# Kernel tuning notes

Measured on AMD Instinct MI355X. Metric: run time of the kernel, lower is better.

## Reference

```python
import jax, jax.numpy as jnp
import numpy as np


def _integral(x):
    # x: [C, H, W] -> summed-area table [C, H+1, W+1] with zero first row/col
    s = jnp.cumsum(jnp.cumsum(x, axis=-2), axis=-1)
    return jnp.pad(s, ((0, 0), (1, 0), (1, 0)))


def _box_sums(S, x0, y0, x1, y1):
    # S: [C, H+1, W+1]; boxes half-open [y0:y1, x0:x1] -> sums [C, N]
    return S[:, y1, x1] - S[:, y0, x1] - S[:, y1, x0] + S[:, y0, x0]


def setup_inputs() -> dict:
    key = jax.random.key(0)
    C, H, W, K, N = 256, 512, 512, 21, 2560
    k1, k2, k3, k4, k5, k6, k7 = jax.random.split(key, 7)
    feature_map = jax.random.normal(k1, (C, H, W), dtype=jnp.float32)
    norm_cam_bg = jax.random.uniform(k2, (K, H, W), dtype=jnp.float32)
    # valid crop boxes (xmin, ymin, xmax, ymax) with 8..64 px extent
    x0 = jax.random.randint(k3, (N,), 0, W - 64)
    y0 = jax.random.randint(k4, (N,), 0, H - 64)
    bw = jax.random.randint(k5, (N,), 8, 64)
    bh = jax.random.randint(k6, (N,), 8, 64)
    boxes = jnp.stack([x0, y0, x0 + bw, y0 + bh], axis=1).astype(jnp.int32)
    labels = jax.random.randint(k7, (N,), 0, K).astype(jnp.int32)
    return {"feature_map": feature_map, "norm_cam_bg": norm_cam_bg,
            "boxes": boxes, "labels": labels}


def reference(feature_map, norm_cam_bg, boxes, labels):
    # feature_map: [C, H, W]; norm_cam_bg: [K, H, W]; boxes: [N, 4] int; labels: [N] int
    K = norm_cam_bg.shape[0]
    N = boxes.shape[0]
    x0, y0, x1, y1 = boxes[:, 0], boxes[:, 1], boxes[:, 2], boxes[:, 3]
    area = ((x1 - x0) * (y1 - y0)).astype(feature_map.dtype)  # [N]

    # per-box adaptive_avg_pool2d(region, (1,1)) == mean over region, via integral image
    S = _integral(feature_map)                                # [C, H+1, W+1]
    pool = _box_sums(S, x0, y0, x1, y1).T / area[:, None]     # [N, C]

    # foreground score: fraction of pixels in box where argmax(CAM) == region label
    cam_predict = jnp.argmax(norm_cam_bg, axis=0)             # [H, W]
    onehot = jax.nn.one_hot(cam_predict, K, dtype=feature_map.dtype)  # [H, W, K]
    Sm = _integral(jnp.moveaxis(onehot, -1, 0))               # [K, H+1, W+1]
    fg_sums = _box_sums(Sm, x0, y0, x1, y1)                   # [K, N]
    fg_score = fg_sums[labels, jnp.arange(N)] / area          # [N]

    return pool, fg_score
```

## Files before the change

### kernel.cpp

```cpp
#include <hip/hip_runtime.h>

#define HWD (512*512)
#define Wd 512
#define Hd 512
#define Cd 256
#define Kd 21
#define Nd 2560
#define NSTRIP 4
#define SROWS 128

__global__ __launch_bounds__(512) void k_events(const int* __restrict__ boxes,
                                                int* __restrict__ ev_start,
                                                unsigned int* __restrict__ ev_list) {
    __shared__ int cnt[512];
    __shared__ int cur[512];
    __shared__ int tt[8];
    const int t = threadIdx.x, lane = t & 63, wv = t >> 6;
    cnt[t] = 0;
    __syncthreads();
    for (int n = t; n < Nd; n += 512) {
        const int y0 = boxes[n * 4 + 1];
        const int y1 = boxes[n * 4 + 3];
        if (y0 > 0) atomicAdd(&cnt[y0 - 1], 1);
        atomicAdd(&cnt[y1 - 1], 1);
    }
    __syncthreads();
    const int v = cnt[t];
    int inc = v;
    #pragma unroll
    for (int d = 1; d < 64; d <<= 1) {
        int u = __shfl_up(inc, d);
        if (lane >= d) inc += u;
    }
    if (lane == 63) tt[wv] = inc;
    __syncthreads();
    int off = 0;
    #pragma unroll
    for (int w = 0; w < 8; ++w) if (w < wv) off += tt[w];
    inc += off;
    cur[t] = inc - v;
    ev_start[t] = inc - v;
    if (t == 511) ev_start[512] = inc;
    __syncthreads();
    for (int n = t; n < Nd; n += 512) {
        const int y0 = boxes[n * 4 + 1];
        const int y1 = boxes[n * 4 + 3];
        if (y0 > 0) {
            const int r = y0 - 1;
            const int p = atomicAdd(&cur[r], 1);
            ev_list[p] = (unsigned)n | ((unsigned)r << 12) | 0x80000000u;
        }
        const int r = y1 - 1;
        const int p = atomicAdd(&cur[r], 1);
        ev_list[p] = (unsigned)n | ((unsigned)r << 12);
    }
}

__global__ __launch_bounds__(512) void k_ipool(const float* __restrict__ f,
                                               const int* __restrict__ boxes,
                                               const int* __restrict__ ev_start,
                                               const unsigned int* __restrict__ ev_list,
                                               float* __restrict__ pool_acc) {
    const int c     = blockIdx.x >> 2;
    const int strip = blockIdx.x & 3;
    const int t = threadIdx.x;
    const int lane = t & 63, wv = t >> 6;
    const float* F = f + (size_t)c * HWD + (size_t)(strip * SROWS) * Wd;

    __shared__ float S[8][512];
    __shared__ float partial[Nd];

    for (int n = t; n < Nd; n += 512) partial[n] = 0.f;

    float colacc = 0.f;
    const float* rp = F + (size_t)wv * Wd + lane * 8;
    float4 a = *(const float4*)(rp);
    float4 b = *(const float4*)(rp + 4);

    for (int yb = 0; yb < SROWS; yb += 8) {
        const bool more = (yb + 8 < SROWS);
        float4 na, nb;
        if (more) {
            const float* np = F + (size_t)(yb + 8 + wv) * Wd + lane * 8;
            na = *(const float4*)(np);
            nb = *(const float4*)(np + 4);
        }

        float v0 = a.x, v1 = v0 + a.y, v2 = v1 + a.z, v3 = v2 + a.w;
        float v4 = v3 + b.x, v5 = v4 + b.y, v6 = v5 + b.z, v7 = v6 + b.w;
        float s = v7, xx = s;
        #pragma unroll
        for (int d = 1; d < 64; d <<= 1) {
            float u = __shfl_up(xx, d);
            if (lane >= d) xx += u;
        }
        const float off = xx - s;
        float4 o0 = { v0 + off, v1 + off, v2 + off, v3 + off };
        float4 o1 = { v4 + off, v5 + off, v6 + off, v7 + off };
        *(float4*)&S[wv][lane * 8]     = o0;
        *(float4*)&S[wv][lane * 8 + 4] = o1;
        __syncthreads();

        #pragma unroll
        for (int j = 0; j < 8; ++j) {
            colacc += S[j][t];
            S[j][t] = colacc;
        }
        __syncthreads();

        const int g0 = strip * SROWS + yb;
        const int e0 = ev_start[g0];
        const int e1 = ev_start[g0 + 8];
        for (int e = e0 + t; e < e1; e += 512) {
            const unsigned ev = ev_list[e];
            const int n  = ev & 0xFFF;
            const int r  = (ev >> 12) & 0x1FF;
            const int x0 = boxes[n * 4 + 0];
            const int x1 = boxes[n * 4 + 2];
            const float sx1 = S[r & 7][x1 - 1];
            const float sx0 = (x0 > 0) ? S[r & 7][x0 - 1] : 0.f;
            const float d = sx1 - sx0;
            partial[n] += (ev & 0x80000000u) ? -d : d;
        }
        __syncthreads();

        if (more) { a = na; b = nb; }
    }

    S[0][t] = colacc;
    __syncthreads();
    for (int n = t; n < Nd; n += 512) {
        const int x0 = boxes[n * 4 + 0];
        const int y0 = boxes[n * 4 + 1];
        const int x1 = boxes[n * 4 + 2];
        const int y1 = boxes[n * 4 + 3];
        float p = partial[n];
        const float tdiff = S[0][x1 - 1] - ((x0 > 0) ? S[0][x0 - 1] : 0.f);
        if (strip < ((y1 - 1) >> 7)) p += tdiff;
        if (y0 > 0 && strip < ((y0 - 1) >> 7)) p -= tdiff;
        pool_acc[((size_t)(strip * Cd + c)) * Nd + n] = p;
    }
}

__global__ __launch_bounds__(512) void k_pool2(const float* __restrict__ pool_acc,
                                               const int* __restrict__ boxes,
                                               float* __restrict__ pool) {
    __shared__ float P[32][257];
    __shared__ float rarea[32];
    const int t = threadIdx.x;
    const int n0 = blockIdx.x * 32;

    if (t < 32) {
        const int x0 = boxes[(n0 + t) * 4 + 0];
        const int y0 = boxes[(n0 + t) * 4 + 1];
        const int x1 = boxes[(n0 + t) * 4 + 2];
        const int y1 = boxes[(n0 + t) * 4 + 3];
        rarea[t] = 1.f / (float)((x1 - x0) * (y1 - y0));
    }

    const int ni = t & 31, ci = t >> 5;
    #pragma unroll
    for (int co = 0; co < 16; ++co) {
        const int c = co * 16 + ci;
        float v = 0.f;
        #pragma unroll
        for (int s = 0; s < NSTRIP; ++s)
            v += pool_acc[((size_t)(s * Cd + c)) * Nd + n0 + ni];
        P[ni][c] = v;
    }
    __syncthreads();

    const int c = t & 255, nn = t >> 8;
    #pragma unroll
    for (int no = 0; no < 16; ++no) {
        const int i = no * 2 + nn;
        pool[(size_t)(n0 + i) * Cd + c] = P[i][c] * rarea[i];
    }
}

__global__ __launch_bounds__(256) void k_argmax(const float* __restrict__ ncb,
                                                unsigned char* __restrict__ map) {
    const int p = blockIdx.x * 256 + threadIdx.x;
    float best = ncb[p];
    int bi = 0;
    #pragma unroll
    for (int k = 1; k < Kd; ++k) {
        float v = ncb[(size_t)k * HWD + p];
        if (v > best) { best = v; bi = k; }
    }
    map[p] = (unsigned char)bi;
}

__global__ __launch_bounds__(256) void k_fg(const unsigned char* __restrict__ map,
                                            const int* __restrict__ boxes,
                                            const int* __restrict__ labels,
                                            float* __restrict__ fg) {
    const int n = blockIdx.x;
    const int x0 = boxes[n * 4 + 0];
    const int y0 = boxes[n * 4 + 1];
    const int x1 = boxes[n * 4 + 2];
    const int y1 = boxes[n * 4 + 3];
    const int lab = labels[n];
    const int lane = threadIdx.x & 63;
    const int wv   = threadIdx.x >> 6;
    const int w = x1 - x0;

    int cnt = 0;
    for (int yy = y0 + wv; yy < y1; yy += 4) {
        if (lane < w)
            cnt += (map[yy * Wd + x0 + lane] == lab) ? 1 : 0;
    }
    #pragma unroll
    for (int d = 32; d; d >>= 1) cnt += __shfl_down(cnt, d);

    __shared__ int sred[4];
    if (lane == 0) sred[wv] = cnt;
    __syncthreads();
    if (threadIdx.x == 0) {
        int tot = sred[0] + sred[1] + sred[2] + sred[3];
        float area = (float)(w * (y1 - y0));
        fg[n] = (float)tot / area;
    }
}

extern "C" void kernel_launch(void* const* d_in, const int* in_sizes, int n_in,
                              void* d_out, int out_size, void* d_ws, size_t ws_size,
                              hipStream_t stream) {
    (void)in_sizes; (void)n_in; (void)out_size; (void)ws_size;

    const float* feature_map = (const float*)d_in[0];
    const float* norm_cam_bg = (const float*)d_in[1];
    const int*   boxes       = (const int*)d_in[2];
    const int*   labels      = (const int*)d_in[3];

    float* out_pool = (float*)d_out;
    float* out_fg   = out_pool + (size_t)Nd * Cd;

    char* ws = (char*)d_ws;
    unsigned char* map      = (unsigned char*)ws;
    int*           ev_start = (int*)(ws + 262144);
    unsigned int*  ev_list  = (unsigned int*)(ws + 266240);
    float*         pool_acc = (float*)(ws + 286720);

    k_events<<<1, 512, 0, stream>>>(boxes, ev_start, ev_list);
    k_argmax<<<HWD / 256, 256, 0, stream>>>(norm_cam_bg, map);
    k_ipool<<<Cd * NSTRIP, 512, 0, stream>>>(feature_map, boxes, ev_start, ev_list,
                                             pool_acc);
    k_pool2<<<Nd / 32, 512, 0, stream>>>(pool_acc, boxes, out_pool);
    k_fg<<<Nd, 256, 0, stream>>>(map, boxes, labels, out_fg);
}
```

Measured before the change: 79.97 us.

## Merge argmax into integral-pool kernel and fg into pool-finalize kernel

The argmax pass now runs as extra blocks of the integral-pool kernel, and the foreground-count pass runs as extra blocks of the pool-finalize kernel, with one box per wave. This cuts five launches to three and lets independent work share the GPU. The pool kernel also drops the in-shared column prefix rewrite and its second barrier per 8-row block. Instead it keeps a double-buffered running column sum and has event threads add up the needed rows themselves, which adds a little per-event work. The launch bound raises the occupancy hint to 8 blocks.

```diff
diff --git a/kernel.cpp b/kernel.cpp
--- a/kernel.cpp
+++ b/kernel.cpp
@@ -56,23 +56,43 @@
     }
 }
 
-__global__ __launch_bounds__(512) void k_ipool(const float* __restrict__ f,
-                                               const int* __restrict__ boxes,
-                                               const int* __restrict__ ev_start,
-                                               const unsigned int* __restrict__ ev_list,
-                                               float* __restrict__ pool_acc) {
-    const int c     = blockIdx.x >> 2;
-    const int strip = blockIdx.x & 3;
+__global__ __launch_bounds__(512, 8) void kA(const float* __restrict__ f,
+                                             const int* __restrict__ boxes,
+                                             const int* __restrict__ ev_start,
+                                             const unsigned int* __restrict__ ev_list,
+                                             const float* __restrict__ ncb,
+                                             unsigned char* __restrict__ map,
+                                             float* __restrict__ pool_acc) {
+    const int bid = blockIdx.x;
     const int t = threadIdx.x;
+
+    if (bid >= Cd * NSTRIP) {
+        const int p = (bid - Cd * NSTRIP) * 512 + t;
+        float best = ncb[p];
+        int bi = 0;
+        #pragma unroll
+        for (int k = 1; k < Kd; ++k) {
+            float v = ncb[(size_t)k * HWD + p];
+            if (v > best) { best = v; bi = k; }
+        }
+        map[p] = (unsigned char)bi;
+        return;
+    }
+
+    const int c     = bid >> 2;
+    const int strip = bid & 3;
     const int lane = t & 63, wv = t >> 6;
     const float* F = f + (size_t)c * HWD + (size_t)(strip * SROWS) * Wd;
 
     __shared__ float S[8][512];
+    __shared__ float C[2][512];
     __shared__ float partial[Nd];
 
     for (int n = t; n < Nd; n += 512) partial[n] = 0.f;
+    C[0][t] = 0.f;
 
     float colacc = 0.f;
+    int buf = 0;
     const float* rp = F + (size_t)wv * Wd + lane * 8;
     float4 a = *(const float4*)(rp);
     float4 b = *(const float4*)(rp + 4);
@@ -101,12 +121,11 @@
         *(float4*)&S[wv][lane * 8 + 4] = o1;
         __syncthreads();
 
-        #pragma unroll
-        for (int j = 0; j < 8; ++j) {
-            colacc += S[j][t];
-            S[j][t] = colacc;
-        }
-        __syncthreads();
+        float cs = 0.f;
+        #pragma unroll
+        for (int j = 0; j < 8; ++j) cs += S[j][t];
+        colacc += cs;
+        C[buf ^ 1][t] = colacc;
 
         const int g0 = strip * SROWS + yb;
         const int e0 = ev_start[g0];
@@ -114,113 +133,95 @@
         for (int e = e0 + t; e < e1; e += 512) {
             const unsigned ev = ev_list[e];
             const int n  = ev & 0xFFF;
-            const int r  = (ev >> 12) & 0x1FF;
+            const int rr = (ev >> 12) & 7;
             const int x0 = boxes[n * 4 + 0];
             const int x1 = boxes[n * 4 + 2];
-            const float sx1 = S[r & 7][x1 - 1];
-            const float sx0 = (x0 > 0) ? S[r & 7][x0 - 1] : 0.f;
+            float sx1 = C[buf][x1 - 1];
+            float sx0 = (x0 > 0) ? C[buf][x0 - 1] : 0.f;
+            for (int j = 0; j <= rr; ++j) {
+                sx1 += S[j][x1 - 1];
+                if (x0 > 0) sx0 += S[j][x0 - 1];
+            }
             const float d = sx1 - sx0;
             partial[n] += (ev & 0x80000000u) ? -d : d;
         }
         __syncthreads();
 
+        buf ^= 1;
         if (more) { a = na; b = nb; }
     }
 
-    S[0][t] = colacc;
-    __syncthreads();
     for (int n = t; n < Nd; n += 512) {
         const int x0 = boxes[n * 4 + 0];
         const int y0 = boxes[n * 4 + 1];
         const int x1 = boxes[n * 4 + 2];
         const int y1 = boxes[n * 4 + 3];
         float p = partial[n];
-        const float tdiff = S[0][x1 - 1] - ((x0 > 0) ? S[0][x0 - 1] : 0.f);
+        const float tdiff = C[buf][x1 - 1] - ((x0 > 0) ? C[buf][x0 - 1] : 0.f);
         if (strip < ((y1 - 1) >> 7)) p += tdiff;
         if (y0 > 0 && strip < ((y0 - 1) >> 7)) p -= tdiff;
         pool_acc[((size_t)(strip * Cd + c)) * Nd + n] = p;
     }
 }
 
-__global__ __launch_bounds__(512) void k_pool2(const float* __restrict__ pool_acc,
-                                               const int* __restrict__ boxes,
-                                               float* __restrict__ pool) {
-    __shared__ float P[32][257];
-    __shared__ float rarea[32];
+__global__ __launch_bounds__(512) void kB(const float* __restrict__ pool_acc,
+                                          const unsigned char* __restrict__ map,
+                                          const int* __restrict__ boxes,
+                                          const int* __restrict__ labels,
+                                          float* __restrict__ pool,
+                                          float* __restrict__ fg) {
+    const int bid = blockIdx.x;
     const int t = threadIdx.x;
-    const int n0 = blockIdx.x * 32;
-
-    if (t < 32) {
-        const int x0 = boxes[(n0 + t) * 4 + 0];
-        const int y0 = boxes[(n0 + t) * 4 + 1];
-        const int x1 = boxes[(n0 + t) * 4 + 2];
-        const int y1 = boxes[(n0 + t) * 4 + 3];
-        rarea[t] = 1.f / (float)((x1 - x0) * (y1 - y0));
-    }
-
-    const int ni = t & 31, ci = t >> 5;
-    #pragma unroll
-    for (int co = 0; co < 16; ++co) {
-        const int c = co * 16 + ci;
-        float v = 0.f;
-        #pragma unroll
-        for (int s = 0; s < NSTRIP; ++s)
-            v += pool_acc[((size_t)(s * Cd + c)) * Nd + n0 + ni];
-        P[ni][c] = v;
-    }
-    __syncthreads();
-
-    const int c = t & 255, nn = t >> 8;
-    #pragma unroll
-    for (int no = 0; no < 16; ++no) {
-        const int i = no * 2 + nn;
-        pool[(size_t)(n0 + i) * Cd + c] = P[i][c] * rarea[i];
-    }
-}
-
-__global__ __launch_bounds__(256) void k_argmax(const float* __restrict__ ncb,
-                                                unsigned char* __restrict__ map) {
-    const int p = blockIdx.x * 256 + threadIdx.x;
-    float best = ncb[p];
-    int bi = 0;
-    #pragma unroll
-    for (int k = 1; k < Kd; ++k) {
-        float v = ncb[(size_t)k * HWD + p];
-        if (v > best) { best = v; bi = k; }
-    }
-    map[p] = (unsigned char)bi;
-}
-
-__global__ __launch_bounds__(256) void k_fg(const unsigned char* __restrict__ map,
-                                            const int* __restrict__ boxes,
-                                            const int* __restrict__ labels,
-                                            float* __restrict__ fg) {
-    const int n = blockIdx.x;
+
+    if (bid < Nd / 32) {
+        __shared__ float P[32][257];
+        __shared__ float rarea[32];
+        const int n0 = bid * 32;
+        if (t < 32) {
+            const int x0 = boxes[(n0 + t) * 4 + 0];
+            const int y0 = boxes[(n0 + t) * 4 + 1];
+            const int x1 = boxes[(n0 + t) * 4 + 2];
+            const int y1 = boxes[(n0 + t) * 4 + 3];
+            rarea[t] = 1.f / (float)((x1 - x0) * (y1 - y0));
+        }
+        const int ni = t & 31, ci = t >> 5;
+        #pragma unroll
+        for (int co = 0; co < 16; ++co) {
+            const int c = co * 16 + ci;
+            float v = 0.f;
+            #pragma unroll
+            for (int s = 0; s < NSTRIP; ++s)
+                v += pool_acc[((size_t)(s * Cd + c)) * Nd + n0 + ni];
+            P[ni][c] = v;
+        }
+        __syncthreads();
+        const int c = t & 255, nn = t >> 8;
+        #pragma unroll
+        for (int no = 0; no < 16; ++no) {
+            const int i = no * 2 + nn;
+            pool[(size_t)(n0 + i) * Cd + c] = P[i][c] * rarea[i];
+        }
+        return;
+    }
+
+    const int lane = t & 63, wv = t >> 6;
+    const int n = (bid - Nd / 32) * 8 + wv;
     const int x0 = boxes[n * 4 + 0];
     const int y0 = boxes[n * 4 + 1];
     const int x1 = boxes[n * 4 + 2];
     const int y1 = boxes[n * 4 + 3];
     const int lab = labels[n];
-    const int lane = threadIdx.x & 63;
-    const int wv   = threadIdx.x >> 6;
     const int w = x1 - x0;
 
     int cnt = 0;
-    for (int yy = y0 + wv; yy < y1; yy += 4) {
+    for (int yy = y0; yy < y1; ++yy) {
         if (lane < w)
             cnt += (map[yy * Wd + x0 + lane] == lab) ? 1 : 0;
     }
     #pragma unroll
     for (int d = 32; d; d >>= 1) cnt += __shfl_down(cnt, d);
-
-    __shared__ int sred[4];
-    if (lane == 0) sred[wv] = cnt;
-    __syncthreads();
-    if (threadIdx.x == 0) {
-        int tot = sred[0] + sred[1] + sred[2] + sred[3];
-        float area = (float)(w * (y1 - y0));
-        fg[n] = (float)tot / area;
-    }
+    if (lane == 0)
+        fg[n] = (float)cnt / (float)(w * (y1 - y0));
 }
 
 extern "C" void kernel_launch(void* const* d_in, const int* in_sizes, int n_in,
@@ -243,9 +244,8 @@
     float*         pool_acc = (float*)(ws + 286720);
 
     k_events<<<1, 512, 0, stream>>>(boxes, ev_start, ev_list);
-    k_argmax<<<HWD / 256, 256, 0, stream>>>(norm_cam_bg, map);
-    k_ipool<<<Cd * NSTRIP, 512, 0, stream>>>(feature_map, boxes, ev_start, ev_list,
-                                             pool_acc);
-    k_pool2<<<Nd / 32, 512, 0, stream>>>(pool_acc, boxes, out_pool);
-    k_fg<<<Nd, 256, 0, stream>>>(map, boxes, labels, out_fg);
-}
+    kA<<<Cd * NSTRIP + HWD / 512, 512, 0, stream>>>(feature_map, boxes, ev_start,
+                                                    ev_list, norm_cam_bg, map, pool_acc);
+    kB<<<Nd / 32 + Nd / 8, 512, 0, stream>>>(pool_acc, map, boxes, labels,
+                                             out_pool, out_fg);
+}
```

After: 89.39 us. 1.12x slower.

## Fuse argmax and event-building kernels; prefetch two row-blocks ahead in ipool

Applied to the files above, without the earlier changes.

Merges the argmax kernel and the single-block event-sorting kernel into one launch, with block 512 doing event construction while the other blocks compute the CAM argmax. This removes one kernel launch and lets the serial event kernel overlap with the argmax work. In the integral-pool kernel the feature rows are now prefetched two 8-row blocks ahead instead of one, to hide more global-load latency at the cost of extra registers. The column-scan reads are also batched into registers before the scan.

```diff
diff --git a/kernel.cpp b/kernel.cpp
--- a/kernel.cpp
+++ b/kernel.cpp
@@ -9,13 +9,29 @@
 #define NSTRIP 4
 #define SROWS 128
 
-__global__ __launch_bounds__(512) void k_events(const int* __restrict__ boxes,
-                                                int* __restrict__ ev_start,
-                                                unsigned int* __restrict__ ev_list) {
+__global__ __launch_bounds__(512) void k_pre(const float* __restrict__ ncb,
+                                             const int* __restrict__ boxes,
+                                             unsigned char* __restrict__ map,
+                                             int* __restrict__ ev_start,
+                                             unsigned int* __restrict__ ev_list) {
+    const int t = threadIdx.x;
+    if (blockIdx.x < 512) {
+        const int p = blockIdx.x * 512 + t;
+        float best = ncb[p];
+        int bi = 0;
+        #pragma unroll
+        for (int k = 1; k < Kd; ++k) {
+            float v = ncb[(size_t)k * HWD + p];
+            if (v > best) { best = v; bi = k; }
+        }
+        map[p] = (unsigned char)bi;
+        return;
+    }
+
     __shared__ int cnt[512];
     __shared__ int cur[512];
     __shared__ int tt[8];
-    const int t = threadIdx.x, lane = t & 63, wv = t >> 6;
+    const int lane = t & 63, wv = t >> 6;
     cnt[t] = 0;
     __syncthreads();
     for (int n = t; n < Nd; n += 512) {
@@ -73,21 +89,25 @@
     for (int n = t; n < Nd; n += 512) partial[n] = 0.f;
 
     float colacc = 0.f;
-    const float* rp = F + (size_t)wv * Wd + lane * 8;
-    float4 a = *(const float4*)(rp);
-    float4 b = *(const float4*)(rp + 4);
+
+    const float* rp0 = F + (size_t)wv * Wd + lane * 8;
+    float4 a0 = *(const float4*)(rp0);
+    float4 b0 = *(const float4*)(rp0 + 4);
+    const float* rp1 = F + (size_t)(8 + wv) * Wd + lane * 8;
+    float4 a1 = *(const float4*)(rp1);
+    float4 b1 = *(const float4*)(rp1 + 4);
 
     for (int yb = 0; yb < SROWS; yb += 8) {
-        const bool more = (yb + 8 < SROWS);
+        const bool more2 = (yb + 16 < SROWS);
         float4 na, nb;
-        if (more) {
-            const float* np = F + (size_t)(yb + 8 + wv) * Wd + lane * 8;
+        if (more2) {
+            const float* np = F + (size_t)(yb + 16 + wv) * Wd + lane * 8;
             na = *(const float4*)(np);
             nb = *(const float4*)(np + 4);
         }
 
-        float v0 = a.x, v1 = v0 + a.y, v2 = v1 + a.z, v3 = v2 + a.w;
-        float v4 = v3 + b.x, v5 = v4 + b.y, v6 = v5 + b.z, v7 = v6 + b.w;
+        float v0 = a0.x, v1 = v0 + a0.y, v2 = v1 + a0.z, v3 = v2 + a0.w;
+        float v4 = v3 + b0.x, v5 = v4 + b0.y, v6 = v5 + b0.z, v7 = v6 + b0.w;
         float s = v7, xx = s;
         #pragma unroll
         for (int d = 1; d < 64; d <<= 1) {
@@ -101,9 +121,12 @@
         *(float4*)&S[wv][lane * 8 + 4] = o1;
         __syncthreads();
 
+        float sv[8];
+        #pragma unroll
+        for (int j = 0; j < 8; ++j) sv[j] = S[j][t];
         #pragma unroll
         for (int j = 0; j < 8; ++j) {
-            colacc += S[j][t];
+            colacc += sv[j];
             S[j][t] = colacc;
         }
         __syncthreads();
@@ -114,17 +137,18 @@
         for (int e = e0 + t; e < e1; e += 512) {
             const unsigned ev = ev_list[e];
             const int n  = ev & 0xFFF;
-            const int r  = (ev >> 12) & 0x1FF;
+            const int rr = (ev >> 12) & 7;
             const int x0 = boxes[n * 4 + 0];
             const int x1 = boxes[n * 4 + 2];
-            const float sx1 = S[r & 7][x1 - 1];
-            const float sx0 = (x0 > 0) ? S[r & 7][x0 - 1] : 0.f;
+            const float sx1 = S[rr][x1 - 1];
+            const float sx0 = (x0 > 0) ? S[rr][x0 - 1] : 0.f;
             const float d = sx1 - sx0;
             partial[n] += (ev & 0x80000000u) ? -d : d;
         }
         __syncthreads();
 
-        if (more) { a = na; b = nb; }
+        a0 = a1; b0 = b1;
+        if (more2) { a1 = na; b1 = nb; }
     }
 
     S[0][t] = colacc;
@@ -176,19 +200,6 @@
         const int i = no * 2 + nn;
         pool[(size_t)(n0 + i) * Cd + c] = P[i][c] * rarea[i];
     }
-}
-
-__global__ __launch_bounds__(256) void k_argmax(const float* __restrict__ ncb,
-                                                unsigned char* __restrict__ map) {
-    const int p = blockIdx.x * 256 + threadIdx.x;
-    float best = ncb[p];
-    int bi = 0;
-    #pragma unroll
-    for (int k = 1; k < Kd; ++k) {
-        float v = ncb[(size_t)k * HWD + p];
-        if (v > best) { best = v; bi = k; }
-    }
-    map[p] = (unsigned char)bi;
 }
 
 __global__ __launch_bounds__(256) void k_fg(const unsigned char* __restrict__ map,
@@ -242,8 +253,7 @@
     unsigned int*  ev_list  = (unsigned int*)(ws + 266240);
     float*         pool_acc = (float*)(ws + 286720);
 
-    k_events<<<1, 512, 0, stream>>>(boxes, ev_start, ev_list);
-    k_argmax<<<HWD / 256, 256, 0, stream>>>(norm_cam_bg, map);
+    k_pre<<<513, 512, 0, stream>>>(norm_cam_bg, boxes, map, ev_start, ev_list);
     k_ipool<<<Cd * NSTRIP, 512, 0, stream>>>(feature_map, boxes, ev_start, ev_list,
                                              pool_acc);
     k_pool2<<<Nd / 32, 512, 0, stream>>>(pool_acc, boxes, out_pool);
```

Result: slower. 81.90 us (+2.4%).
